# Kernel optimization log

Hardware: AMD Instinct MI355X
Metric: run time of the kernel (lower is better)

Reference implementation:

```python
import jax, jax.numpy as jnp
import numpy as np

NUM_REL = 5
NUM_BASES = 8
HID = 128
OUT = 64
IN_FEAT = 256
N_PER_TYPE = 50000
N_NODES = 2 * N_PER_TYPE
N_EDGES = 1000000
EPS = 1e-5  # PairNorm eps


def setup_inputs() -> dict:
    key = jax.random.key(0)
    ks = jax.random.split(key, 14)
    inp = {
        "x_author": jax.random.normal(ks[0], (N_PER_TYPE, IN_FEAT), jnp.float32),
        "x_paper": jax.random.normal(ks[1], (N_PER_TYPE, IN_FEAT), jnp.float32),
        "edge_index": jax.random.randint(ks[2], (2, N_EDGES), 0, N_NODES, jnp.int32),
        "edge_type": jax.random.randint(ks[3], (N_EDGES,), 0, NUM_REL, jnp.int32),
        # per-node-type input projections (nn.Linear)
        "proj_author_w": jax.random.normal(ks[4], (IN_FEAT, HID), jnp.float32) / np.sqrt(IN_FEAT),
        "proj_author_b": jnp.zeros((HID,), jnp.float32),
        "proj_paper_w": jax.random.normal(ks[5], (IN_FEAT, HID), jnp.float32) / np.sqrt(IN_FEAT),
        "proj_paper_b": jnp.zeros((HID,), jnp.float32),
        # RGCNConv layer 0 (hidden -> hidden), basis decomposition, root weight, no bias
        "comp0": jax.random.normal(ks[6], (NUM_REL, NUM_BASES), jnp.float32) / np.sqrt(NUM_BASES),
        "basis0": jax.random.normal(ks[7], (NUM_BASES, HID, HID), jnp.float32) / np.sqrt(HID),
        "root0": jax.random.normal(ks[8], (HID, HID), jnp.float32) / np.sqrt(HID),
        # RGCNConv layer 1 (hidden -> out)
        "comp1": jax.random.normal(ks[9], (NUM_REL, NUM_BASES), jnp.float32) / np.sqrt(NUM_BASES),
        "basis1": jax.random.normal(ks[10], (NUM_BASES, HID, OUT), jnp.float32) / np.sqrt(HID),
        "root1": jax.random.normal(ks[11], (HID, OUT), jnp.float32) / np.sqrt(HID),
    }
    return inp


def pairnorm(x):
    # PyG PairNorm (scale=1, scale_individually=False)
    x = x - x.mean(axis=0, keepdims=True)
    return x / jnp.sqrt(EPS + (x * x).sum(-1).mean())


def rgcn_conv(x, edge_index, edge_type, comp, basis, root):
    # weight[r] = sum_b comp[r,b] * basis[b]  -> [R, Fin, Fout]
    W = jnp.einsum('rb,bio->rio', comp, basis)
    src, dst = edge_index[0], edge_index[1]
    msgs = x[src]                                   # [E, Fin] gather
    seg = dst * NUM_REL + edge_type                 # per (node, relation) segment
    agg = jax.ops.segment_sum(msgs, seg, num_segments=N_NODES * NUM_REL)
    agg = agg.reshape(N_NODES, NUM_REL, -1)         # [N, R, Fin]
    cnt = jax.ops.segment_sum(jnp.ones((msgs.shape[0],), x.dtype), seg,
                              num_segments=N_NODES * NUM_REL).reshape(N_NODES, NUM_REL)
    mean = agg / jnp.maximum(cnt, 1.0)[..., None]   # mean aggregation (0 if no edges)
    return jnp.einsum('nrf,rfo->no', mean, W) + x @ root


def reference(x_author, x_paper, edge_index, edge_type,
              proj_author_w, proj_author_b, proj_paper_w, proj_paper_b,
              comp0, basis0, root0, comp1, basis1, root1):
    h_a = jax.nn.relu(x_author @ proj_author_w + proj_author_b)
    h_p = jax.nn.relu(x_paper @ proj_paper_w + proj_paper_b)
    x = jnp.concatenate([h_a, h_p], axis=0)         # [N, HID]
    x = jax.nn.relu(rgcn_conv(x, edge_index, edge_type, comp0, basis0, root0))
    x = pairnorm(x)
    x_latent = x
    x = rgcn_conv(x, edge_index, edge_type, comp1, basis1, root1)
    x = pairnorm(x)
    return (x, x_latent)
```

## Files before the change

kernel.cpp:

```cpp
#include <hip/hip_runtime.h>
#include <hip/hip_bf16.h>

constexpr int NPT    = 50000;
constexpr int NN     = 100000;
constexpr int NE     = 1000000;
constexpr int HID    = 128;
constexpr int OUTF   = 64;
constexpr int INF    = 256;
constexpr int NREL   = 5;
constexpr int NSEG   = NN * NREL;

typedef __attribute__((ext_vector_type(8))) short short8v;
typedef __attribute__((ext_vector_type(4))) float f32x4;

__device__ __forceinline__ ushort f2bf(float x) {
    uint u = __builtin_bit_cast(uint, x);
    uint r = (u + 0x7FFFu + ((u >> 16) & 1u)) >> 16;
    return (ushort)r;
}
__device__ __forceinline__ float bfhi(uint raw) {
    return __builtin_bit_cast(float, raw & 0xFFFF0000u);
}
__device__ __forceinline__ float bflo(uint raw) {
    return __builtin_bit_cast(float, raw << 16);
}

__device__ __forceinline__ void build_wbT_body(const float* __restrict__ comp,
                                               const float* __restrict__ basis,
                                               const float* __restrict__ root,
                                               ushort* __restrict__ wbT,
                                               int fout, int passOff, int idx) {
    int col = idx >> 7, k = idx & 127;
    float v;
    if (col < 320) {
        int r = col >> 6, f = (col & 63) + passOff;
        v = 0.f;
#pragma unroll
        for (int b = 0; b < 8; b++)
            v += comp[r * 8 + b] * basis[(b * 128 + k) * fout + f];
    } else {
        v = root[k * fout + (col - 320) + passOff];
    }
    wbT[col * 128 + k] = f2bf(v);
}

__global__ void prep_kernel(const float* __restrict__ comp0, const float* __restrict__ basis0,
                            const float* __restrict__ root0,
                            const float* __restrict__ comp1, const float* __restrict__ basis1,
                            const float* __restrict__ root1,
                            const float* __restrict__ paw, const float* __restrict__ ppw,
                            ushort* __restrict__ wbT0a, ushort* __restrict__ wbT0b,
                            ushort* __restrict__ wbT1,
                            ushort* __restrict__ wpa, ushort* __restrict__ wpp,
                            int* __restrict__ cnt, float* __restrict__ pnscr,
                            int* __restrict__ recs_pad) {
    const int b = blockIdx.x, t = threadIdx.x;
    if (b < 1954) {
        int i = b * 256 + t;
        if (i < NSEG) cnt[i] = 0;
    } else if (b < 1956) {
        pnscr[(b - 1954) * 256 + t] = 0.f;
    } else if (b == 1956) {
        if (t < 128) recs_pad[t] = 0;
    } else if (b < 2149) {
        build_wbT_body(comp0, basis0, root0, wbT0a, HID, 0, (b - 1957) * 256 + t);
    } else if (b < 2341) {
        build_wbT_body(comp0, basis0, root0, wbT0b, HID, 64, (b - 2149) * 256 + t);
    } else if (b < 2533) {
        build_wbT_body(comp1, basis1, root1, wbT1, OUTF, 0, (b - 2341) * 256 + t);
    } else if (b < 2661) {
        int i = (b - 2533) * 256 + t;
        wpa[(size_t)(i & 127) * 256 + (i >> 7)] = f2bf(paw[i]);
    } else {
        int i = (b - 2661) * 256 + t;
        wpp[(size_t)(i & 127) * 256 + (i >> 7)] = f2bf(ppw[i]);
    }
}

__launch_bounds__(256)
__global__ void proj_mfma(const float* __restrict__ xa, const float* __restrict__ xp,
                          const ushort* __restrict__ wTa, const ushort* __restrict__ wTp,
                          const float* __restrict__ ba, const float* __restrict__ bp,
                          ushort* __restrict__ x0b) {
    __shared__ ushort sx[16][264];
    __shared__ ushort so[16][132];
    const int tid = threadIdx.x;
    const bool author = blockIdx.x < 625;
    const int tile0 = (blockIdx.x - (author ? 0 : 625)) * 5;
    const float* x = author ? xa : xp;
    const ushort* wT = author ? wTa : wTp;
    const float* bias = author ? ba : bp;
    const int typeBase = author ? 0 : NPT;

    const int wave = tid >> 6, lane = tid & 63;
    const int row = lane & 15, g = lane >> 4;
    const int fcol = wave * 32 + row;

    const ushort* wp0 = wT + (size_t)fcol * 256 + g * 8;
    short8v bA[8], bB[8];
#pragma unroll
    for (int kk = 0; kk < 8; kk++) bA[kk] = *(const short8v*)&wp0[kk * 32];
#pragma unroll
    for (int kk = 0; kk < 8; kk++) bB[kk] = *(const short8v*)&wp0[16 * 256 + kk * 32];
    const float bv0 = bias[fcol], bv1 = bias[fcol + 16];

    const int sr = tid >> 4, part = tid & 15;
    const int fnode = tid >> 4, fb = (tid & 15) * 8;

    for (int t = 0; t < 5; t++) {
        const int nloc = (tile0 + t) * 16;
        {
            size_t rowoff = (size_t)(nloc + sr) * INF + part * 16;
#pragma unroll
            for (int ii = 0; ii < 4; ii++) {
                float4 v = *(const float4*)&x[rowoff + ii * 4];
                ushort4 h = {f2bf(v.x), f2bf(v.y), f2bf(v.z), f2bf(v.w)};
                *(ushort4*)&sx[sr][part * 16 + ii * 4] = h;
            }
        }
        __syncthreads();
        short8v a[8];
#pragma unroll
        for (int kk = 0; kk < 8; kk++) a[kk] = *(const short8v*)&sx[row][kk * 32 + g * 8];
        {
            f32x4 acc0 = {0.f, 0.f, 0.f, 0.f};
            f32x4 acc1 = {0.f, 0.f, 0.f, 0.f};
#pragma unroll
            for (int kk = 0; kk < 8; kk++) {
                acc0 = __builtin_amdgcn_mfma_f32_16x16x32_bf16(a[kk], bA[kk], acc0, 0, 0, 0);
                acc1 = __builtin_amdgcn_mfma_f32_16x16x32_bf16(a[kk], bB[kk], acc1, 0, 0, 0);
            }
#pragma unroll
            for (int q = 0; q < 4; q++) {
                so[g * 4 + q][fcol]      = f2bf(fmaxf(acc0[q] + bv0, 0.f));
                so[g * 4 + q][fcol + 16] = f2bf(fmaxf(acc1[q] + bv1, 0.f));
            }
        }
        __syncthreads();
        {
            ushort4 v0 = *(const ushort4*)&so[fnode][fb];
            ushort4 v1 = *(const ushort4*)&so[fnode][fb + 4];
            size_t gbase = (size_t)(typeBase + nloc + fnode) * 128 + fb;
            *(ushort4*)&x0b[gbase] = v0;
            *(ushort4*)&x0b[gbase + 4] = v1;
        }
    }
}

__global__ void hist_kernel(const int* __restrict__ ei, const int* __restrict__ et,
                            int* __restrict__ cnt, int* __restrict__ rank) {
    int e = blockIdx.x * blockDim.x + threadIdx.x;
    if (e < NE) {
        int seg = ei[NE + e] * NREL + et[e];
        rank[e] = atomicAdd(&cnt[seg], 1);
    }
}

__global__ void scan1(const int* __restrict__ cnt, int* __restrict__ offs,
                      int* __restrict__ bsums, int n) {
    __shared__ int lds[256];
    const int t = threadIdx.x;
    const int base = blockIdx.x * 2048 + t * 8;
    int vals[8];
    int s = 0;
#pragma unroll
    for (int v = 0; v < 8; v++) {
        int idx = base + v;
        vals[v] = (idx < n) ? cnt[idx] : 0;
        s += vals[v];
    }
    lds[t] = s;
    __syncthreads();
    for (int off = 1; off < 256; off <<= 1) {
        int x = lds[t];
        int y = (t >= off) ? lds[t - off] : 0;
        __syncthreads();
        lds[t] = x + y;
        __syncthreads();
    }
    int run = (t > 0) ? lds[t - 1] : 0;
    if (t == 255) bsums[blockIdx.x] = lds[255];
#pragma unroll
    for (int v = 0; v < 8; v++) {
        int idx = base + v;
        if (idx < n) offs[idx] = run;
        run += vals[v];
    }
}

__global__ void scan2(const int* __restrict__ bsums, int* __restrict__ bsums2, int nb) {
    __shared__ int lds[256];
    const int t = threadIdx.x;
    lds[t] = (t < nb) ? bsums[t] : 0;
    __syncthreads();
    for (int off = 1; off < 256; off <<= 1) {
        int x = lds[t];
        int y = (t >= off) ? lds[t - off] : 0;
        __syncthreads();
        lds[t] = x + y;
        __syncthreads();
    }
    if (t < nb) bsums2[t] = (t > 0) ? lds[t - 1] : 0;
}

__global__ void scan3_desc(const int* __restrict__ offs, const int* __restrict__ bsums2,
                           const int* __restrict__ cnt, int2* __restrict__ desc, int n) {
    int i = blockIdx.x * blockDim.x + threadIdx.x;
    if (i < n) {
        int2 d = {offs[i] + bsums2[i >> 11], cnt[i]};
        desc[i] = d;
    }
}

__global__ void scatter_kernel(const int* __restrict__ ei, const int* __restrict__ et,
                               const int* __restrict__ rank,
                               const int2* __restrict__ desc, int2* __restrict__ recs) {
    int e = blockIdx.x * blockDim.x + threadIdx.x;
    if (e < NE) {
        int src = ei[e];
        int dst = ei[NE + e];
        int r = et[e];
        int2 d = desc[dst * NREL + r];
        int c = d.y;
        float sc = 1.f / (float)((c > 1) ? c : 1);
        int2 rec = {r * NN + src, __builtin_bit_cast(int, sc)};
        recs[d.x + rank[e]] = rec;
    }
}

__launch_bounds__(256)
__global__ void ytab_gemm(const ushort* __restrict__ xin, const ushort* __restrict__ wbT,
                          ushort* __restrict__ ytab, float* __restrict__ hout,
                          int ytabW, int outStride, int outOff) {
    __shared__ ushort sx[32][136];
    __shared__ ushort so[32][328];
    __shared__ float sroot[32][68];
    const int tid = threadIdx.x;
    const int tile0 = blockIdx.x * 5;
    const int wave = tid >> 6, lane = tid & 63;
    const int row = lane & 15, g = lane >> 4;
    const int wbase = wave * 96;

    const ushort* wp = wbT + (size_t)(wbase + row) * 128 + g * 8;
    short8v B[6][4];
#pragma unroll
    for (int t = 0; t < 6; t++)
#pragma unroll
        for (int kk = 0; kk < 4; kk++)
            B[t][kk] = *(const short8v*)&wp[t * 2048 + kk * 32];

    const int sr = tid >> 3, sc = (tid & 7) * 16;
    const int fnode = tid >> 3, fb = (tid & 7) * 8;

    for (int tt = 0; tt < 5; tt++) {
        const int n0 = (tile0 + tt) * 32;
        {
            const ushort* src = &xin[(size_t)(n0 + sr) * 128 + sc];
            *(short8v*)&sx[sr][sc] = *(const short8v*)&src[0];
            *(short8v*)&sx[sr][sc + 8] = *(const short8v*)&src[8];
        }
        __syncthreads();

        short8v a[2][4];
#pragma unroll
        for (int m = 0; m < 2; m++)
#pragma unroll
            for (int kk = 0; kk < 4; kk++)
                a[m][kk] = *(const short8v*)&sx[m * 16 + row][kk * 32 + g * 8];

#pragma unroll
        for (int t = 0; t < 6; t++) {
            f32x4 acc0 = {0.f, 0.f, 0.f, 0.f};
            f32x4 acc1 = {0.f, 0.f, 0.f, 0.f};
#pragma unroll
            for (int kk = 0; kk < 4; kk++) {
                acc0 = __builtin_amdgcn_mfma_f32_16x16x32_bf16(a[0][kk], B[t][kk], acc0, 0, 0, 0);
                acc1 = __builtin_amdgcn_mfma_f32_16x16x32_bf16(a[1][kk], B[t][kk], acc1, 0, 0, 0);
            }
            const int col = wbase + t * 16 + row;
            if (col < 320) {
#pragma unroll
                for (int q = 0; q < 4; q++) {
                    so[g * 4 + q][col] = f2bf(acc0[q]);
                    so[16 + g * 4 + q][col] = f2bf(acc1[q]);
                }
            } else {
                const int f = col - 320;
#pragma unroll
                for (int q = 0; q < 4; q++) {
                    sroot[g * 4 + q][f] = acc0[q];
                    sroot[16 + g * 4 + q][f] = acc1[q];
                }
            }
        }
        __syncthreads();

        {
#pragma unroll
            for (int r = 0; r < NREL; r++) {
                short8v v = *(const short8v*)&so[fnode][r * 64 + fb];
                *(short8v*)&ytab[(size_t)r * NN * ytabW + (size_t)(n0 + fnode) * ytabW
                                 + outOff + fb] = v;
            }
            float4 r0 = *(const float4*)&sroot[fnode][fb];
            float4 r1 = *(const float4*)&sroot[fnode][fb + 4];
            float* hp = &hout[(size_t)(n0 + fnode) * outStride + outOff + fb];
            *(float4*)&hp[0] = r0;
            *(float4*)&hp[4] = r1;
        }
    }
}

template <int FW>
__launch_bounds__(256)
__global__ void agg_kernel(const ushort* __restrict__ ytab,
                           const int2* __restrict__ recs,
                           const int2* __restrict__ desc,
                           float* __restrict__ hout) {
    const int tid = threadIdx.x;
    const int wave = tid >> 6, lane = tid & 63;
    const int half = lane >> 5, fl = lane & 31;
    const int n0 = blockIdx.x * 16 + wave * 4;

    int start[4], total[4];
#pragma unroll
    for (int rep = 0; rep < 4; rep++) {
        const int s5 = (n0 + rep) * NREL;
        int2 d0 = desc[s5];
        int2 d4 = desc[s5 + 4];
        start[rep] = d0.x;
        total[rep] = d4.x + d4.y - d0.x;
    }
    int2 rec[4];
#pragma unroll
    for (int rep = 0; rep < 4; rep++) rec[rep] = recs[start[rep] + lane];

    constexpr int FPL = FW / 32;
    float hpre[4][FPL];
#pragma unroll
    for (int rep = 0; rep < 4; rep++) {
        const float* hp = &hout[(size_t)(n0 + rep) * FW + fl * FPL];
#pragma unroll
        for (int q = 0; q < FPL; q++) hpre[rep][q] = hp[q];
    }

#pragma unroll
    for (int rep = 0; rep < 4; rep++) {
        if (total[rep] <= 0) continue;
        float acc[FPL];
#pragma unroll
        for (int q = 0; q < FPL; q++) acc[q] = 0.f;
        const int lim = (total[rep] > 64) ? 64 : total[rep];
#pragma unroll 2
        for (int j2 = half; j2 < lim; j2 += 2) {
            int rw = __shfl(rec[rep].x, j2);
            float sc = __builtin_bit_cast(float, __shfl(rec[rep].y, j2));
            if (FW == 128) {
                uint2 raw = *(const uint2*)&ytab[(size_t)rw * FW + fl * 4];
                acc[0] += sc * bflo(raw.x);
                acc[1] += sc * bfhi(raw.x);
                acc[2] += sc * bflo(raw.y);
                acc[3] += sc * bfhi(raw.y);
            } else {
                uint raw = *(const uint*)&ytab[(size_t)rw * FW + fl * 2];
                acc[0] += sc * bflo(raw);
                acc[1] += sc * bfhi(raw);
            }
        }
        if (total[rep] > 64) {
            for (int j = 64 + half; j < total[rep]; j += 2) {
                int2 r2 = recs[start[rep] + j];
                float sc = __builtin_bit_cast(float, r2.y);
                if (FW == 128) {
                    uint2 raw = *(const uint2*)&ytab[(size_t)r2.x * FW + fl * 4];
                    acc[0] += sc * bflo(raw.x);
                    acc[1] += sc * bfhi(raw.x);
                    acc[2] += sc * bflo(raw.y);
                    acc[3] += sc * bfhi(raw.y);
                } else {
                    uint raw = *(const uint*)&ytab[(size_t)r2.x * FW + fl * 2];
                    acc[0] += sc * bflo(raw);
                    acc[1] += sc * bfhi(raw);
                }
            }
        }
#pragma unroll
        for (int q = 0; q < FPL; q++) acc[q] += __shfl_xor(acc[q], 32);
        if (half == 0) {
            float* hp = &hout[(size_t)(n0 + rep) * FW + fl * FPL];
            float o[FPL];
#pragma unroll
            for (int q = 0; q < FPL; q++) o[q] = hpre[rep][q] + acc[q];
            if (FW == 128) *(float4*)hp = *(float4*)o;
            else           *(float2*)hp = *(float2*)o;
        }
    }
}

template <int F, bool RELU>
__global__ void stats_kernel(const float* __restrict__ x, float* __restrict__ colsum,
                             float* __restrict__ sumsq) {
    constexpr int NSUB = 256 / F;
    const int f = threadIdx.x & (F - 1);
    const int sub = threadIdx.x / F;
    float cs = 0.f, ss = 0.f;
    const int stride = gridDim.x * NSUB;
    for (int n = blockIdx.x * NSUB + sub; n < NN; n += stride) {
        float v = x[(size_t)n * F + f];
        if (RELU) v = fmaxf(v, 0.f);
        cs += v;
        ss += v * v;
    }
    __shared__ float sred[256];
    sred[threadIdx.x] = cs;
    __syncthreads();
    if (sub == 0) {
        float t = cs;
#pragma unroll
        for (int s2 = 1; s2 < NSUB; s2++) t += sred[s2 * F + f];
        atomicAdd(&colsum[f], t);
    }
    __syncthreads();
    sred[threadIdx.x] = ss;
    __syncthreads();
    for (int h = 128; h > 0; h >>= 1) {
        if (threadIdx.x < h) sred[threadIdx.x] += sred[threadIdx.x + h];
        __syncthreads();
    }
    if (threadIdx.x == 0) atomicAdd(sumsq, sred[0]);
}

template <int F>
__global__ void finalize_kernel(const float* __restrict__ colsum,
                                const float* __restrict__ sumsq,
                                float* __restrict__ mu_inv) {
    __shared__ float sred[128];
    const int f = threadIdx.x;
    float mu = colsum[f] / (float)NN;
    mu_inv[f] = mu;
    sred[f] = mu * mu;
    __syncthreads();
    for (int h = F / 2; h > 0; h >>= 1) {
        if (f < h) sred[f] += sred[f + h];
        __syncthreads();
    }
    if (f == 0) {
        float var = sumsq[0] / (float)NN - sred[0];
        mu_inv[F] = rsqrtf(1e-5f + var);
    }
}

__global__ void normalize_dual(const float* __restrict__ x,
                               const float* __restrict__ mu_inv,
                               float* __restrict__ outf, ushort* __restrict__ outb,
                               int total4) {
    int i = blockIdx.x * blockDim.x + threadIdx.x;
    if (i < total4) {
        int base = i * 4;
        int f = base & 127;
        float4 v = *(const float4*)&x[base];
        float4 m = *(const float4*)&mu_inv[f];
        float s = mu_inv[128];
        float4 o = {(fmaxf(v.x, 0.f) - m.x) * s, (fmaxf(v.y, 0.f) - m.y) * s,
                    (fmaxf(v.z, 0.f) - m.z) * s, (fmaxf(v.w, 0.f) - m.w) * s};
        *(float4*)&outf[base] = o;
        ushort4 h = {f2bf(o.x), f2bf(o.y), f2bf(o.z), f2bf(o.w)};
        *(ushort4*)&outb[base] = h;
    }
}

template <int F>
__global__ void normalize_kernel(const float* __restrict__ x,
                                 const float* __restrict__ mu_inv,
                                 float* __restrict__ out, int total4) {
    int i = blockIdx.x * blockDim.x + threadIdx.x;
    if (i < total4) {
        int base = i * 4;
        int f = base & (F - 1);
        float4 v = *(const float4*)&x[base];
        float4 m = *(const float4*)&mu_inv[f];
        float s = mu_inv[F];
        float4 o = {(v.x - m.x) * s, (v.y - m.y) * s, (v.z - m.z) * s, (v.w - m.w) * s};
        *(float4*)&out[base] = o;
    }
}

extern "C" void kernel_launch(void* const* d_in, const int* in_sizes, int n_in,
                              void* d_out, int out_size, void* d_ws, size_t ws_size,
                              hipStream_t stream) {
    const float* xa    = (const float*)d_in[0];
    const float* xp    = (const float*)d_in[1];
    const int*   ei    = (const int*)d_in[2];
    const int*   et    = (const int*)d_in[3];
    const float* paw   = (const float*)d_in[4];
    const float* pab   = (const float*)d_in[5];
    const float* ppw   = (const float*)d_in[6];
    const float* ppb   = (const float*)d_in[7];
    const float* comp0 = (const float*)d_in[8];
    const float* basis0= (const float*)d_in[9];
    const float* root0 = (const float*)d_in[10];
    const float* comp1 = (const float*)d_in[11];
    const float* basis1= (const float*)d_in[12];
    const float* root1 = (const float*)d_in[13];
    float* out = (float*)d_out;

    char* ws = (char*)d_ws;
    size_t o = 0;
    auto alloc = [&](size_t b) { size_t p = o; o += (b + 255) & ~(size_t)255; return p; };
    ushort* x0b   = (ushort*)(ws + alloc((size_t)NN * HID * 2));
    ushort* xlatb = (ushort*)(ws + alloc((size_t)NN * HID * 2));
    ushort* ytab  = (ushort*)(ws + alloc((size_t)NREL * NN * 128 * 2));
    int2*   desc  = (int2*)(ws + alloc((size_t)NSEG * 8));
    int2*   recs  = (int2*)(ws + alloc((size_t)(NE + 64) * 8));
    ushort* wbT0a = (ushort*)(ws + alloc(384 * 128 * 2));
    ushort* wbT0b = (ushort*)(ws + alloc(384 * 128 * 2));
    ushort* wbT1  = (ushort*)(ws + alloc(384 * 128 * 2));
    ushort* wpa   = (ushort*)(ws + alloc(128 * 256 * 2));
    ushort* wpp   = (ushort*)(ws + alloc(128 * 256 * 2));
    float*  pnscr = (float*)(ws + alloc(512 * 4));
    float*  mu0   = (float*)(ws + alloc(129 * 4));
    float*  mu1   = (float*)(ws + alloc(65 * 4));
    float *cs0 = pnscr, *ss0 = pnscr + 128, *cs1 = pnscr + 192, *ss1 = pnscr + 256;

    char* ybase = (char*)ytab;
    int* cnt    = (int*)(ybase);
    int* offs   = (int*)(ybase + (size_t)NSEG * 4);
    int* rank   = (int*)(ybase + (size_t)NSEG * 8);
    int* bsums  = (int*)(ybase + (size_t)NSEG * 8 + (size_t)NE * 4);
    int* bsums2 = (int*)(ybase + (size_t)NSEG * 8 + (size_t)NE * 4 + 4096);

    float* h0 = out + (size_t)NN * OUTF;
    float* h1 = out;
    float* xlat = h0;

    prep_kernel<<<2789, 256, 0, stream>>>(comp0, basis0, root0, comp1, basis1, root1,
                                          paw, ppw, wbT0a, wbT0b, wbT1, wpa, wpp,
                                          cnt, pnscr, (int*)(recs + NE));
    proj_mfma<<<1250, 256, 0, stream>>>(xa, xp, wpa, wpp, pab, ppb, x0b);

    hist_kernel<<<(NE + 255) / 256, 256, 0, stream>>>(ei, et, cnt, rank);
    const int nb = (NSEG + 2047) / 2048;
    scan1<<<nb, 256, 0, stream>>>(cnt, offs, bsums, NSEG);
    scan2<<<1, 256, 0, stream>>>(bsums, bsums2, nb);
    scan3_desc<<<(NSEG + 255) / 256, 256, 0, stream>>>(offs, bsums2, cnt, desc, NSEG);
    scatter_kernel<<<(NE + 255) / 256, 256, 0, stream>>>(ei, et, rank, desc, recs);

    ytab_gemm<<<625, 256, 0, stream>>>(x0b, wbT0a, ytab, h0, 128, HID, 0);
    ytab_gemm<<<625, 256, 0, stream>>>(x0b, wbT0b, ytab, h0, 128, HID, 64);
    agg_kernel<128><<<NN / 16, 256, 0, stream>>>(ytab, recs, desc, h0);
    stats_kernel<HID, true><<<512, 256, 0, stream>>>(h0, cs0, ss0);
    finalize_kernel<HID><<<1, HID, 0, stream>>>(cs0, ss0, mu0);
    normalize_dual<<<(NN * HID / 4 + 255) / 256, 256, 0, stream>>>(h0, mu0, xlat, xlatb,
                                                                   NN * HID / 4);

    ytab_gemm<<<625, 256, 0, stream>>>(xlatb, wbT1, ytab, h1, 64, OUTF, 0);
    agg_kernel<64><<<NN / 16, 256, 0, stream>>>(ytab, recs, desc, h1);
    stats_kernel<OUTF, false><<<512, 256, 0, stream>>>(h1, cs1, ss1);
    finalize_kernel<OUTF><<<1, OUTF, 0, stream>>>(cs1, ss1, mu1);
    normalize_kernel<OUTF><<<(NN * OUTF / 4 + 255) / 256, 256, 0, stream>>>(h1, mu1, out,
                                                                            NN * OUTF / 4);
}
```

Baseline: 425.2 us.

## Fuse PairNorm stats into aggregation, normalize into next GEMM, merge launches

Column sums and sums of squares for PairNorm are now accumulated inside the aggregation kernel and reduced into 32 replicated atomic slots, which removes the separate stats pass over the hidden features. The layer-0 normalize step is folded into the layer-1 GEMM's load stage, which writes the normalized fp32 latent in place and builds the bf16 operand on the fly. The edge histogram runs as extra blocks of the projection kernel, and the two layer-0 GEMM halves share one launch. Together these cut kernel launches and full-array passes, at the cost of more atomics and more work per thread in agg and gemm1.

```diff
diff --git a/kernel.cpp b/kernel.cpp
--- a/kernel.cpp
+++ b/kernel.cpp
@@ -52,39 +52,49 @@
                             ushort* __restrict__ wbT0a, ushort* __restrict__ wbT0b,
                             ushort* __restrict__ wbT1,
                             ushort* __restrict__ wpa, ushort* __restrict__ wpp,
-                            int* __restrict__ cnt, float* __restrict__ pnscr,
+                            int* __restrict__ cnt, float* __restrict__ statscr,
                             int* __restrict__ recs_pad) {
     const int b = blockIdx.x, t = threadIdx.x;
     if (b < 1954) {
         int i = b * 256 + t;
         if (i < NSEG) cnt[i] = 0;
-    } else if (b < 1956) {
-        pnscr[(b - 1954) * 256 + t] = 0.f;
-    } else if (b == 1956) {
+    } else if (b < 1979) {
+        statscr[(b - 1954) * 256 + t] = 0.f;
+    } else if (b == 1979) {
         if (t < 128) recs_pad[t] = 0;
-    } else if (b < 2149) {
-        build_wbT_body(comp0, basis0, root0, wbT0a, HID, 0, (b - 1957) * 256 + t);
-    } else if (b < 2341) {
-        build_wbT_body(comp0, basis0, root0, wbT0b, HID, 64, (b - 2149) * 256 + t);
-    } else if (b < 2533) {
-        build_wbT_body(comp1, basis1, root1, wbT1, OUTF, 0, (b - 2341) * 256 + t);
-    } else if (b < 2661) {
-        int i = (b - 2533) * 256 + t;
+    } else if (b < 2172) {
+        build_wbT_body(comp0, basis0, root0, wbT0a, HID, 0, (b - 1980) * 256 + t);
+    } else if (b < 2364) {
+        build_wbT_body(comp0, basis0, root0, wbT0b, HID, 64, (b - 2172) * 256 + t);
+    } else if (b < 2556) {
+        build_wbT_body(comp1, basis1, root1, wbT1, OUTF, 0, (b - 2364) * 256 + t);
+    } else if (b < 2684) {
+        int i = (b - 2556) * 256 + t;
         wpa[(size_t)(i & 127) * 256 + (i >> 7)] = f2bf(paw[i]);
     } else {
-        int i = (b - 2661) * 256 + t;
+        int i = (b - 2684) * 256 + t;
         wpp[(size_t)(i & 127) * 256 + (i >> 7)] = f2bf(ppw[i]);
     }
 }
 
 __launch_bounds__(256)
-__global__ void proj_mfma(const float* __restrict__ xa, const float* __restrict__ xp,
+__global__ void proj_hist(const float* __restrict__ xa, const float* __restrict__ xp,
                           const ushort* __restrict__ wTa, const ushort* __restrict__ wTp,
                           const float* __restrict__ ba, const float* __restrict__ bp,
-                          ushort* __restrict__ x0b) {
+                          ushort* __restrict__ x0b,
+                          const int* __restrict__ ei, const int* __restrict__ et,
+                          int* __restrict__ cnt, int* __restrict__ rank) {
     __shared__ ushort sx[16][264];
     __shared__ ushort so[16][132];
     const int tid = threadIdx.x;
+    if (blockIdx.x >= 1250) {
+        int e = (blockIdx.x - 1250) * 256 + tid;
+        if (e < NE) {
+            int seg = ei[NE + e] * NREL + et[e];
+            rank[e] = atomicAdd(&cnt[seg], 1);
+        }
+        return;
+    }
     const bool author = blockIdx.x < 625;
     const int tile0 = (blockIdx.x - (author ? 0 : 625)) * 5;
     const float* x = author ? xa : xp;
@@ -144,15 +154,6 @@
             *(ushort4*)&x0b[gbase] = v0;
             *(ushort4*)&x0b[gbase + 4] = v1;
         }
-    }
-}
-
-__global__ void hist_kernel(const int* __restrict__ ei, const int* __restrict__ et,
-                            int* __restrict__ cnt, int* __restrict__ rank) {
-    int e = blockIdx.x * blockDim.x + threadIdx.x;
-    if (e < NE) {
-        int seg = ei[NE + e] * NREL + et[e];
-        rank[e] = atomicAdd(&cnt[seg], 1);
     }
 }
 
@@ -229,9 +230,95 @@
 }
 
 __launch_bounds__(256)
-__global__ void ytab_gemm(const ushort* __restrict__ xin, const ushort* __restrict__ wbT,
-                          ushort* __restrict__ ytab, float* __restrict__ hout,
-                          int ytabW, int outStride, int outOff) {
+__global__ void ytab_gemm0(const ushort* __restrict__ xin,
+                           const ushort* __restrict__ wbT_a, const ushort* __restrict__ wbT_b,
+                           ushort* __restrict__ ytab, float* __restrict__ hout) {
+    __shared__ ushort sx[32][136];
+    __shared__ ushort so[32][328];
+    __shared__ float sroot[32][68];
+    const int tid = threadIdx.x;
+    const bool first = blockIdx.x < 625;
+    const int tile0 = (first ? blockIdx.x : blockIdx.x - 625) * 5;
+    const ushort* wbT = first ? wbT_a : wbT_b;
+    const int outOff = first ? 0 : 64;
+    const int wave = tid >> 6, lane = tid & 63;
+    const int row = lane & 15, g = lane >> 4;
+    const int wbase = wave * 96;
+
+    const ushort* wp = wbT + (size_t)(wbase + row) * 128 + g * 8;
+    short8v B[6][4];
+#pragma unroll
+    for (int t = 0; t < 6; t++)
+#pragma unroll
+        for (int kk = 0; kk < 4; kk++)
+            B[t][kk] = *(const short8v*)&wp[t * 2048 + kk * 32];
+
+    const int sr = tid >> 3, scl = (tid & 7) * 16;
+    const int fnode = tid >> 3, fb = (tid & 7) * 8;
+
+    for (int tt = 0; tt < 5; tt++) {
+        const int n0 = (tile0 + tt) * 32;
+        {
+            const ushort* src = &xin[(size_t)(n0 + sr) * 128 + scl];
+            *(short8v*)&sx[sr][scl] = *(const short8v*)&src[0];
+            *(short8v*)&sx[sr][scl + 8] = *(const short8v*)&src[8];
+        }
+        __syncthreads();
+
+        short8v a[2][4];
+#pragma unroll
+        for (int m = 0; m < 2; m++)
+#pragma unroll
+            for (int kk = 0; kk < 4; kk++)
+                a[m][kk] = *(const short8v*)&sx[m * 16 + row][kk * 32 + g * 8];
+
+#pragma unroll
+        for (int t = 0; t < 6; t++) {
+            f32x4 acc0 = {0.f, 0.f, 0.f, 0.f};
+            f32x4 acc1 = {0.f, 0.f, 0.f, 0.f};
+#pragma unroll
+            for (int kk = 0; kk < 4; kk++) {
+                acc0 = __builtin_amdgcn_mfma_f32_16x16x32_bf16(a[0][kk], B[t][kk], acc0, 0, 0, 0);
+                acc1 = __builtin_amdgcn_mfma_f32_16x16x32_bf16(a[1][kk], B[t][kk], acc1, 0, 0, 0);
+            }
+            const int col = wbase + t * 16 + row;
+            if (col < 320) {
+#pragma unroll
+                for (int q = 0; q < 4; q++) {
+                    so[g * 4 + q][col] = f2bf(acc0[q]);
+                    so[16 + g * 4 + q][col] = f2bf(acc1[q]);
+                }
+            } else {
+                const int f = col - 320;
+#pragma unroll
+                for (int q = 0; q < 4; q++) {
+                    sroot[g * 4 + q][f] = acc0[q];
+                    sroot[16 + g * 4 + q][f] = acc1[q];
+                }
+            }
+        }
+        __syncthreads();
+
+        {
+#pragma unroll
+            for (int r = 0; r < NREL; r++) {
+                short8v v = *(const short8v*)&so[fnode][r * 64 + fb];
+                *(short8v*)&ytab[(size_t)r * NN * 128 + (size_t)(n0 + fnode) * 128
+                                 + outOff + fb] = v;
+            }
+            float4 r0 = *(const float4*)&sroot[fnode][fb];
+            float4 r1 = *(const float4*)&sroot[fnode][fb + 4];
+            float* hp = &hout[(size_t)(n0 + fnode) * HID + outOff + fb];
+            *(float4*)&hp[0] = r0;
+            *(float4*)&hp[4] = r1;
+        }
+    }
+}
+
+__launch_bounds__(256)
+__global__ void ytab_gemm1(float* __restrict__ h0x, const float* __restrict__ mu,
+                           const ushort* __restrict__ wbT,
+                           ushort* __restrict__ ytab, float* __restrict__ h1) {
     __shared__ ushort sx[32][136];
     __shared__ ushort so[32][328];
     __shared__ float sroot[32][68];
@@ -249,24 +336,46 @@
         for (int kk = 0; kk < 4; kk++)
             B[t][kk] = *(const short8v*)&wp[t * 2048 + kk * 32];
 
-    const int sr = tid >> 3, sc = (tid & 7) * 16;
+    const int sr = tid >> 3, scl = (tid & 7) * 16;
     const int fnode = tid >> 3, fb = (tid & 7) * 8;
+
+    float m[16];
+#pragma unroll
+    for (int i = 0; i < 16; i++) m[i] = mu[scl + i];
+    const float s = mu[128];
 
     for (int tt = 0; tt < 5; tt++) {
         const int n0 = (tile0 + tt) * 32;
         {
-            const ushort* src = &xin[(size_t)(n0 + sr) * 128 + sc];
-            *(short8v*)&sx[sr][sc] = *(const short8v*)&src[0];
-            *(short8v*)&sx[sr][sc + 8] = *(const short8v*)&src[8];
+            float* hp = &h0x[(size_t)(n0 + sr) * 128 + scl];
+            float v[16];
+#pragma unroll
+            for (int i = 0; i < 4; i++) {
+                float4 t4 = *(const float4*)&hp[i * 4];
+                v[i * 4 + 0] = (t4.x - m[i * 4 + 0]) * s;
+                v[i * 4 + 1] = (t4.y - m[i * 4 + 1]) * s;
+                v[i * 4 + 2] = (t4.z - m[i * 4 + 2]) * s;
+                v[i * 4 + 3] = (t4.w - m[i * 4 + 3]) * s;
+            }
+            ushort hb[16];
+#pragma unroll
+            for (int i = 0; i < 16; i++) hb[i] = f2bf(v[i]);
+#pragma unroll
+            for (int i = 0; i < 4; i++) {
+                float4 t4 = {v[i * 4], v[i * 4 + 1], v[i * 4 + 2], v[i * 4 + 3]};
+                *(float4*)&hp[i * 4] = t4;
+            }
+            *(short8v*)&sx[sr][scl] = *(const short8v*)&hb[0];
+            *(short8v*)&sx[sr][scl + 8] = *(const short8v*)&hb[8];
         }
         __syncthreads();
 
         short8v a[2][4];
 #pragma unroll
-        for (int m = 0; m < 2; m++)
+        for (int mi = 0; mi < 2; mi++)
 #pragma unroll
             for (int kk = 0; kk < 4; kk++)
-                a[m][kk] = *(const short8v*)&sx[m * 16 + row][kk * 32 + g * 8];
+                a[mi][kk] = *(const short8v*)&sx[mi * 16 + row][kk * 32 + g * 8];
 
 #pragma unroll
         for (int t = 0; t < 6; t++) {
@@ -299,24 +408,26 @@
 #pragma unroll
             for (int r = 0; r < NREL; r++) {
                 short8v v = *(const short8v*)&so[fnode][r * 64 + fb];
-                *(short8v*)&ytab[(size_t)r * NN * ytabW + (size_t)(n0 + fnode) * ytabW
-                                 + outOff + fb] = v;
+                *(short8v*)&ytab[(size_t)r * NN * 64 + (size_t)(n0 + fnode) * 64 + fb] = v;
             }
             float4 r0 = *(const float4*)&sroot[fnode][fb];
             float4 r1 = *(const float4*)&sroot[fnode][fb + 4];
-            float* hp = &hout[(size_t)(n0 + fnode) * outStride + outOff + fb];
+            float* hp = &h1[(size_t)(n0 + fnode) * OUTF + fb];
             *(float4*)&hp[0] = r0;
             *(float4*)&hp[4] = r1;
         }
     }
 }
 
-template <int FW>
+template <int FW, bool RELU>
 __launch_bounds__(256)
 __global__ void agg_kernel(const ushort* __restrict__ ytab,
                            const int2* __restrict__ recs,
                            const int2* __restrict__ desc,
-                           float* __restrict__ hout) {
+                           float* __restrict__ hout,
+                           float* __restrict__ csrep, float* __restrict__ ssrep) {
+    constexpr int FPL = FW / 32;
+    __shared__ float sred[4][32][FPL + 1];
     const int tid = threadIdx.x;
     const int wave = tid >> 6, lane = tid & 63;
     const int half = lane >> 5, fl = lane & 31;
@@ -333,9 +444,11 @@
     }
     int2 rec[4];
 #pragma unroll
-    for (int rep = 0; rep < 4; rep++) rec[rep] = recs[start[rep] + lane];
-
-    constexpr int FPL = FW / 32;
+    for (int rep = 0; rep < 4; rep++) {
+        rec[rep].x = 0; rec[rep].y = 0;
+        if (lane < total[rep]) rec[rep] = recs[start[rep] + lane];
+    }
+
     float hpre[4][FPL];
 #pragma unroll
     for (int rep = 0; rep < 4; rep++) {
@@ -344,9 +457,13 @@
         for (int q = 0; q < FPL; q++) hpre[rep][q] = hp[q];
     }
 
+    float cs_loc[FPL];
+#pragma unroll
+    for (int q = 0; q < FPL; q++) cs_loc[q] = 0.f;
+    float ss_loc = 0.f;
+
 #pragma unroll
     for (int rep = 0; rep < 4; rep++) {
-        if (total[rep] <= 0) continue;
         float acc[FPL];
 #pragma unroll
         for (int q = 0; q < FPL; q++) acc[q] = 0.f;
@@ -387,56 +504,51 @@
 #pragma unroll
         for (int q = 0; q < FPL; q++) acc[q] += __shfl_xor(acc[q], 32);
         if (half == 0) {
+            float o[FPL];
+#pragma unroll
+            for (int q = 0; q < FPL; q++) {
+                o[q] = hpre[rep][q] + acc[q];
+                if (RELU) o[q] = fmaxf(o[q], 0.f);
+                cs_loc[q] += o[q];
+                ss_loc += o[q] * o[q];
+            }
             float* hp = &hout[(size_t)(n0 + rep) * FW + fl * FPL];
-            float o[FPL];
-#pragma unroll
-            for (int q = 0; q < FPL; q++) o[q] = hpre[rep][q] + acc[q];
             if (FW == 128) *(float4*)hp = *(float4*)o;
             else           *(float2*)hp = *(float2*)o;
         }
     }
-}
-
-template <int F, bool RELU>
-__global__ void stats_kernel(const float* __restrict__ x, float* __restrict__ colsum,
-                             float* __restrict__ sumsq) {
-    constexpr int NSUB = 256 / F;
-    const int f = threadIdx.x & (F - 1);
-    const int sub = threadIdx.x / F;
-    float cs = 0.f, ss = 0.f;
-    const int stride = gridDim.x * NSUB;
-    for (int n = blockIdx.x * NSUB + sub; n < NN; n += stride) {
-        float v = x[(size_t)n * F + f];
-        if (RELU) v = fmaxf(v, 0.f);
-        cs += v;
-        ss += v * v;
-    }
-    __shared__ float sred[256];
-    sred[threadIdx.x] = cs;
+
+    if (half == 0) {
+#pragma unroll
+        for (int q = 0; q < FPL; q++) sred[wave][fl][q] = cs_loc[q];
+        sred[wave][fl][FPL] = ss_loc;
+    }
     __syncthreads();
-    if (sub == 0) {
-        float t = cs;
-#pragma unroll
-        for (int s2 = 1; s2 < NSUB; s2++) t += sred[s2 * F + f];
-        atomicAdd(&colsum[f], t);
-    }
-    __syncthreads();
-    sred[threadIdx.x] = ss;
-    __syncthreads();
-    for (int h = 128; h > 0; h >>= 1) {
-        if (threadIdx.x < h) sred[threadIdx.x] += sred[threadIdx.x + h];
-        __syncthreads();
-    }
-    if (threadIdx.x == 0) atomicAdd(sumsq, sred[0]);
+    if (tid < 32) {
+        float sq[FPL + 1];
+#pragma unroll
+        for (int q = 0; q <= FPL; q++)
+            sq[q] = sred[0][tid][q] + sred[1][tid][q] + sred[2][tid][q] + sred[3][tid][q];
+        const int repl = blockIdx.x & 31;
+#pragma unroll
+        for (int q = 0; q < FPL; q++)
+            atomicAdd(&csrep[repl * FW + tid * FPL + q], sq[q]);
+        float ssv = sq[FPL];
+#pragma unroll
+        for (int mof = 16; mof > 0; mof >>= 1) ssv += __shfl_xor(ssv, mof);
+        if (tid == 0) atomicAdd(&ssrep[repl], ssv);
+    }
 }
 
 template <int F>
-__global__ void finalize_kernel(const float* __restrict__ colsum,
-                                const float* __restrict__ sumsq,
-                                float* __restrict__ mu_inv) {
+__global__ void finalize_rep(const float* __restrict__ csrep,
+                             const float* __restrict__ ssrep,
+                             float* __restrict__ mu_inv) {
     __shared__ float sred[128];
     const int f = threadIdx.x;
-    float mu = colsum[f] / (float)NN;
+    float s = 0.f;
+    for (int r = 0; r < 32; r++) s += csrep[r * F + f];
+    float mu = s / (float)NN;
     mu_inv[f] = mu;
     sred[f] = mu * mu;
     __syncthreads();
@@ -445,27 +557,10 @@
         __syncthreads();
     }
     if (f == 0) {
-        float var = sumsq[0] / (float)NN - sred[0];
+        float ss = 0.f;
+        for (int r = 0; r < 32; r++) ss += ssrep[r];
+        float var = ss / (float)NN - sred[0];
         mu_inv[F] = rsqrtf(1e-5f + var);
-    }
-}
-
-__global__ void normalize_dual(const float* __restrict__ x,
-                               const float* __restrict__ mu_inv,
-                               float* __restrict__ outf, ushort* __restrict__ outb,
-                               int total4) {
-    int i = blockIdx.x * blockDim.x + threadIdx.x;
-    if (i < total4) {
-        int base = i * 4;
-        int f = base & 127;
-        float4 v = *(const float4*)&x[base];
-        float4 m = *(const float4*)&mu_inv[f];
-        float s = mu_inv[128];
-        float4 o = {(fmaxf(v.x, 0.f) - m.x) * s, (fmaxf(v.y, 0.f) - m.y) * s,
-                    (fmaxf(v.z, 0.f) - m.z) * s, (fmaxf(v.w, 0.f) - m.w) * s};
-        *(float4*)&outf[base] = o;
-        ushort4 h = {f2bf(o.x), f2bf(o.y), f2bf(o.z), f2bf(o.w)};
-        *(ushort4*)&outb[base] = h;
     }
 }
 
@@ -507,20 +602,22 @@
     char* ws = (char*)d_ws;
     size_t o = 0;
     auto alloc = [&](size_t b) { size_t p = o; o += (b + 255) & ~(size_t)255; return p; };
-    ushort* x0b   = (ushort*)(ws + alloc((size_t)NN * HID * 2));
-    ushort* xlatb = (ushort*)(ws + alloc((size_t)NN * HID * 2));
-    ushort* ytab  = (ushort*)(ws + alloc((size_t)NREL * NN * 128 * 2));
-    int2*   desc  = (int2*)(ws + alloc((size_t)NSEG * 8));
-    int2*   recs  = (int2*)(ws + alloc((size_t)(NE + 64) * 8));
-    ushort* wbT0a = (ushort*)(ws + alloc(384 * 128 * 2));
-    ushort* wbT0b = (ushort*)(ws + alloc(384 * 128 * 2));
-    ushort* wbT1  = (ushort*)(ws + alloc(384 * 128 * 2));
-    ushort* wpa   = (ushort*)(ws + alloc(128 * 256 * 2));
-    ushort* wpp   = (ushort*)(ws + alloc(128 * 256 * 2));
-    float*  pnscr = (float*)(ws + alloc(512 * 4));
-    float*  mu0   = (float*)(ws + alloc(129 * 4));
-    float*  mu1   = (float*)(ws + alloc(65 * 4));
-    float *cs0 = pnscr, *ss0 = pnscr + 128, *cs1 = pnscr + 192, *ss1 = pnscr + 256;
+    ushort* x0b    = (ushort*)(ws + alloc((size_t)NN * HID * 2));
+    ushort* ytab   = (ushort*)(ws + alloc((size_t)NREL * NN * 128 * 2));
+    int2*   desc   = (int2*)(ws + alloc((size_t)NSEG * 8));
+    int2*   recs   = (int2*)(ws + alloc((size_t)(NE + 64) * 8));
+    ushort* wbT0a  = (ushort*)(ws + alloc(384 * 128 * 2));
+    ushort* wbT0b  = (ushort*)(ws + alloc(384 * 128 * 2));
+    ushort* wbT1   = (ushort*)(ws + alloc(384 * 128 * 2));
+    ushort* wpa    = (ushort*)(ws + alloc(128 * 256 * 2));
+    ushort* wpp    = (ushort*)(ws + alloc(128 * 256 * 2));
+    float*  statscr= (float*)(ws + alloc(6400 * 4));
+    float*  mu0    = (float*)(ws + alloc(129 * 4));
+    float*  mu1    = (float*)(ws + alloc(65 * 4));
+    float* cs0rep = statscr;
+    float* ss0rep = statscr + 4096;
+    float* cs1rep = statscr + 4128;
+    float* ss1rep = statscr + 6176;
 
     char* ybase = (char*)ytab;
     int* cnt    = (int*)(ybase);
@@ -531,32 +628,26 @@
 
     float* h0 = out + (size_t)NN * OUTF;
     float* h1 = out;
-    float* xlat = h0;
-
-    prep_kernel<<<2789, 256, 0, stream>>>(comp0, basis0, root0, comp1, basis1, root1,
+
+    prep_kernel<<<2812, 256, 0, stream>>>(comp0, basis0, root0, comp1, basis1, root1,
                                           paw, ppw, wbT0a, wbT0b, wbT1, wpa, wpp,
-                                          cnt, pnscr, (int*)(recs + NE));
-    proj_mfma<<<1250, 256, 0, stream>>>(xa, xp, wpa, wpp, pab, ppb, x0b);
-
-    hist_kernel<<<(NE + 255) / 256, 256, 0, stream>>>(ei, et, cnt, rank);
+                                          cnt, statscr, (int*)(recs + NE));
+    proj_hist<<<1250 + (NE + 255) / 256, 256, 0, stream>>>(xa, xp, wpa, wpp, pab, ppb,
+                                                           x0b, ei, et, cnt, rank);
+
     const int nb = (NSEG + 2047) / 2048;
     scan1<<<nb, 256, 0, stream>>>(cnt, offs, bsums, NSEG);
     scan2<<<1, 256, 0, stream>>>(bsums, bsums2, nb);
     scan3_desc<<<(NSEG + 255) / 256, 256, 0, stream>>>(offs, bsums2, cnt, desc, NSEG);
     scatter_kernel<<<(NE + 255) / 256, 256, 0, stream>>>(ei, et, rank, desc, recs);
 
-    ytab_gemm<<<625, 256, 0, stream>>>(x0b, wbT0a, ytab, h0, 128, HID, 0);
-    ytab_gemm<<<625, 256, 0, stream>>>(x0b, wbT0b, ytab, h0, 128, HID, 64);
-    agg_kernel<128><<<NN / 16, 256, 0, stream>>>(ytab, recs, desc, h0);
-    stats_kernel<HID, true><<<512, 256, 0, stream>>>(h0, cs0, ss0);
-    finalize_kernel<HID><<<1, HID, 0, stream>>>(cs0, ss0, mu0);
-    normalize_dual<<<(NN * HID / 4 + 255) / 256, 256, 0, stream>>>(h0, mu0, xlat, xlatb,
-                                                                   NN * HID / 4);
-
-    ytab_gemm<<<625, 256, 0, stream>>>(xlatb, wbT1, ytab, h1, 64, OUTF, 0);
-    agg_kernel<64><<<NN / 16, 256, 0, stream>>>(ytab, recs, desc, h1);
-    stats_kernel<OUTF, false><<<512, 256, 0, stream>>>(h1, cs1, ss1);
-    finalize_kernel<OUTF><<<1, OUTF, 0, stream>>>(cs1, ss1, mu1);
+    ytab_gemm0<<<1250, 256, 0, stream>>>(x0b, wbT0a, wbT0b, ytab, h0);
+    agg_kernel<128, true><<<NN / 16, 256, 0, stream>>>(ytab, recs, desc, h0, cs0rep, ss0rep);
+    finalize_rep<128><<<1, 128, 0, stream>>>(cs0rep, ss0rep, mu0);
+
+    ytab_gemm1<<<625, 256, 0, stream>>>(h0, mu0, wbT1, ytab, h1);
+    agg_kernel<64, false><<<NN / 16, 256, 0, stream>>>(ytab, recs, desc, h1, cs1rep, ss1rep);
+    finalize_rep<64><<<1, 64, 0, stream>>>(cs1rep, ss1rep, mu1);
     normalize_kernel<OUTF><<<(NN * OUTF / 4 + 255) / 256, 256, 0, stream>>>(h1, mu1, out,
                                                                             NN * OUTF / 4);
 }
```

Result: faster. 364.3 us (-14.3%).
